# Kernel optimization log

Measured on AMD Instinct MI355X. Metric: run time of the kernel, lower is better.

The kernel has to match this reference:

```python
import jax, jax.numpy as jnp
from jax import lax
import numpy as np

B, L_IN, C_IN, C_MARK = 4, 1024, 7, 4
D, H, DK, DFF, NL = 512, 8, 64, 2048, 4
WINDOW = [4, 4, 4]
INNER = 5


def _get_mask(input_size, window_size, inner_size):
    all_size = [input_size]
    for w in window_size:
        all_size.append(all_size[-1] // w)
    L = sum(all_size)
    m = np.zeros((L, L), dtype=np.float32)
    iw = inner_size // 2
    for li in range(len(all_size)):
        start = sum(all_size[:li])
        for i in range(start, start + all_size[li]):
            m[i, max(i - iw, start):min(i + iw + 1, start + all_size[li])] = 1
    for li in range(1, len(all_size)):
        start = sum(all_size[:li])
        for i in range(start, start + all_size[li]):
            ls = start - all_size[li - 1] + (i - start) * window_size[li - 1]
            if i == start + all_size[li] - 1:
                rs = start
            else:
                rs = start - all_size[li - 1] + (i - start + 1) * window_size[li - 1]
            m[i, ls:rs] = 1
            m[ls:rs, i] = 1
    return (1 - m).astype(bool), all_size


def _refer_points(all_sizes, window_size):
    n = all_sizes[0]
    idx = np.zeros((n, len(all_sizes)), dtype=np.int64)
    for i in range(n):
        idx[i, 0] = i
        former = i
        for j in range(1, len(all_sizes)):
            start = sum(all_sizes[:j])
            inner = former - (start - all_sizes[j - 1])
            former = start + min(inner // window_size[j - 1], all_sizes[j] - 1)
            idx[i, j] = former
    return idx


def _pos_emb(L, d):
    pos = np.arange(L, dtype=np.float32)[:, None]
    div = np.exp(np.arange(0, d, 2, dtype=np.float32) * (-np.log(10000.0) / d))
    pe = np.zeros((L, d), dtype=np.float32)
    pe[:, 0::2] = np.sin(pos * div)
    pe[:, 1::2] = np.cos(pos * div)
    return pe


def _ln(x, g, b, eps=1e-5):
    mu = x.mean(-1, keepdims=True)
    v = ((x - mu) ** 2).mean(-1, keepdims=True)
    return (x - mu) * lax.rsqrt(v + eps) * g + b


def setup_inputs() -> dict:
    key = jax.random.key(0)
    ks = iter(jax.random.split(key, 64))

    def nrm(shape, fan_in):
        return jax.random.normal(next(ks), shape, jnp.float32) / np.float32(np.sqrt(fan_in))

    return dict(
        x_enc=jax.random.normal(next(ks), (B, L_IN, C_IN), jnp.float32),
        x_mark=jax.random.uniform(next(ks), (B, L_IN, C_MARK), jnp.float32),
        conv_w=nrm((D, C_IN, 3), C_IN * 3), conv_b=jnp.zeros((D,), jnp.float32),
        temp_w=nrm((C_MARK, D), C_MARK), temp_b=jnp.zeros((D,), jnp.float32),
        down_w=nrm((D, DK), D), down_b=jnp.zeros((DK,), jnp.float32),
        pyr_conv_w=nrm((3, DK, DK, WINDOW[0]), DK * WINDOW[0]),
        pyr_conv_b=jnp.zeros((3, DK), jnp.float32),
        bn_g=jnp.ones((3, DK), jnp.float32), bn_b=jnp.zeros((3, DK), jnp.float32),
        up_w=nrm((DK, D), DK), up_b=jnp.zeros((D,), jnp.float32),
        norm_g=jnp.ones((D,), jnp.float32), norm_b=jnp.zeros((D,), jnp.float32),
        wq=nrm((NL, D, H * DK), D), wk=nrm((NL, D, H * DK), D), wv=nrm((NL, D, H * DK), D),
        fc_w=nrm((NL, H * DK, D), H * DK), fc_b=jnp.zeros((NL, D), jnp.float32),
        ln1_g=jnp.ones((NL, D), jnp.float32), ln1_b=jnp.zeros((NL, D), jnp.float32),
        w1=nrm((NL, D, DFF), D), b1=jnp.zeros((NL, DFF), jnp.float32),
        w2=nrm((NL, DFF, D), DFF), b2=jnp.zeros((NL, D), jnp.float32),
        ln2_g=jnp.ones((NL, D), jnp.float32), ln2_b=jnp.zeros((NL, D), jnp.float32),
    )


def reference(x_enc, x_mark, conv_w, conv_b, temp_w, temp_b, down_w, down_b,
              pyr_conv_w, pyr_conv_b, bn_g, bn_b, up_w, up_b, norm_g, norm_b,
              wq, wk, wv, fc_w, fc_b, ln1_g, ln1_b, w1, b1, w2, b2, ln2_g, ln2_b):
    mask_np, all_size = _get_mask(L_IN, WINDOW, INNER)
    mask = jnp.asarray(mask_np)                      # (L_tot, L_tot) bool, True = blocked
    idx = jnp.asarray(_refer_points(all_size, WINDOW))  # (L_IN, n_levels)
    pe = jnp.asarray(_pos_emb(L_IN, D))
    L_tot = sum(all_size)

    # --- DataEmbedding: circular Conv1d token emb + positional + temporal linear ---
    xt = jnp.transpose(x_enc, (0, 2, 1))             # (B, C_IN, L)
    xt = jnp.concatenate([xt[:, :, -1:], xt, xt[:, :, :1]], axis=-1)  # circular pad=1
    val = lax.conv_general_dilated(xt, conv_w, (1,), 'VALID',
                                   dimension_numbers=('NCH', 'OIH', 'NCH'))
    val = jnp.transpose(val, (0, 2, 1)) + conv_b
    seq = val + pe[None] + x_mark @ temp_w + temp_b  # (B, L_IN, D); dropout = eval no-op

    # --- Bottleneck_Construct: build pyramid levels with strided convs ---
    tmp = jnp.transpose(seq @ down_w + down_b, (0, 2, 1))  # (B, DK, L_IN)
    outs = []
    for i in range(len(WINDOW)):
        tmp = lax.conv_general_dilated(tmp, pyr_conv_w[i], (WINDOW[i],), 'VALID',
                                       dimension_numbers=('NCH', 'OIH', 'NCH'))
        tmp = tmp + pyr_conv_b[i][None, :, None]
        # BatchNorm1d at eval with running stats (0,1): affine only
        tmp = jax.nn.elu(tmp * bn_g[i][None, :, None] + bn_b[i][None, :, None])
        outs.append(tmp)
    pyr = jnp.transpose(jnp.concatenate(outs, axis=2), (0, 2, 1)) @ up_w + up_b
    seq = _ln(jnp.concatenate([seq, pyr], axis=1), norm_g, norm_b)  # (B, L_tot, D)

    temperature = float(np.sqrt(DK))
    for l in range(NL):
        # post-norm multi-head attention with pyramidal boolean mask
        res = seq
        q = (seq @ wq[l]).reshape(B, L_tot, H, DK)
        k = (seq @ wk[l]).reshape(B, L_tot, H, DK)
        v = (seq @ wv[l]).reshape(B, L_tot, H, DK)
        att = jnp.einsum('bqhd,bkhd->bhqk', q / temperature, k)
        att = jnp.where(mask[None, None], jnp.float32(-1e9), att)
        p = jax.nn.softmax(att, axis=-1)
        o = jnp.einsum('bhqk,bkhd->bqhd', p, v).reshape(B, L_tot, H * DK)
        seq = _ln(o @ fc_w[l] + fc_b[l] + res, ln1_g[l], ln1_b[l])
        # post-norm FFN (exact gelu, as F.gelu)
        res = seq
        hmid = jax.nn.gelu(seq @ w1[l] + b1[l], approximate=False)
        seq = _ln(hmid @ w2[l] + b2[l] + res, ln2_g[l], ln2_b[l])

    # --- refer_points gather: concat all pyramid levels per input position ---
    out = seq[:, idx, :]                             # (B, L_IN, n_levels, D)
    return out.reshape(B, L_IN, -1)                  # (B, L_IN, n_levels*D)
```

## Files before the change

kernel.cpp:

```cpp
#include <hip/hip_runtime.h>
#include <hip/hip_bf16.h>
#include <math.h>


typedef __attribute__((ext_vector_type(8))) short short8;
typedef __attribute__((ext_vector_type(4))) float f32x4;

__device__ inline ushort f2bf(float x) {
  union { __hip_bfloat16 h; ushort u; } cv; cv.h = __float2bfloat16(x); return cv.u;
}
__device__ inline float bf2f(ushort u) {
  union { unsigned int i; float f; } cv; cv.i = (unsigned)u << 16; return cv.f;
}
__device__ inline float lo16(unsigned u) { union { unsigned i; float f; } c; c.i = u << 16; return c.f; }
__device__ inline float hi16(unsigned u) { union { unsigned i; float f; } c; c.i = u & 0xffff0000u; return c.f; }
__device__ inline unsigned pack2(float a, float b) {
  return (unsigned)f2bf(a) | ((unsigned)f2bf(b) << 16);
}

__device__ inline float gelu_f(float x) {
  float y = 0.7978845608028654f * (x + 0.044715f * x * x * x);
  float t = __expf(-2.0f * y);
  float th = (1.0f - t) / (1.0f + t);
  return 0.5f * x * (1.0f + th);
}

__device__ inline int xcd_chunk(int orig, int nwg) {
  int q = nwg >> 3, r = nwg & 7;
  int xcd = orig & 7, idx = orig >> 3;
  int base = (xcd < r) ? xcd * (q + 1) : r * (q + 1) + (xcd - r) * q;
  return base + idx;
}

#define GLD16(gp, lp)                                                        \
  __builtin_amdgcn_global_load_lds(                                          \
      (const __attribute__((address_space(1))) void*)(gp),                   \
      (__attribute__((address_space(3))) void*)(lp), 16, 0, 0)

__global__ __launch_bounds__(512) void embed_kernel(
    const float* __restrict__ x_enc, const float* __restrict__ x_mark,
    const float* __restrict__ conv_w, const float* __restrict__ conv_b,
    const float* __restrict__ temp_w, const float* __restrict__ temp_b,
    float* __restrict__ e, ushort* __restrict__ e_bf) {
  int bl = blockIdx.x;
  int b = bl >> 10, l = bl & 1023;
  int d = threadIdx.x;
  int lm1 = (l + 1023) & 1023;
  int lp1 = (l + 1) & 1023;
  const float* w  = conv_w + d * 21;
  const float* x0 = x_enc + (size_t)(b * 1024 + lm1) * 7;
  const float* x1 = x_enc + (size_t)(b * 1024 + l)   * 7;
  const float* x2 = x_enc + (size_t)(b * 1024 + lp1) * 7;
  float acc = conv_b[d];
#pragma unroll
  for (int ci = 0; ci < 7; ci++) {
    acc = fmaf(x0[ci], w[ci * 3 + 0], acc);
    acc = fmaf(x1[ci], w[ci * 3 + 1], acc);
    acc = fmaf(x2[ci], w[ci * 3 + 2], acc);
  }
  int j = d >> 1;
  float dv = __expf((float)(2 * j) * (-9.210340371976184f / 512.0f));
  float ang = (float)l * dv;
  float pe = (d & 1) ? __cosf(ang) : __sinf(ang);
  const float* xm = x_mark + (size_t)(b * 1024 + l) * 4;
  float mk = temp_b[d];
  mk = fmaf(xm[0], temp_w[d],        mk);
  mk = fmaf(xm[1], temp_w[512 + d],  mk);
  mk = fmaf(xm[2], temp_w[1024 + d], mk);
  mk = fmaf(xm[3], temp_w[1536 + d], mk);
  float v = acc + pe + mk;
  e[(size_t)bl * 512 + d] = v;
  e_bf[(size_t)bl * 512 + d] = f2bf(v);
}

__global__ __launch_bounds__(256) void transpose_cast(
    const float* __restrict__ src, ushort* __restrict__ dst,
    int K, int N, size_t src_lstride, size_t dst_lstride) {
  src += (size_t)blockIdx.z * src_lstride;
  dst += (size_t)blockIdx.z * dst_lstride;
  __shared__ float t[32][33];
  int k0 = blockIdx.y * 32, n0 = blockIdx.x * 32;
  int tx = threadIdx.x, ty = threadIdx.y;
#pragma unroll
  for (int i = 0; i < 4; i++)
    t[ty + i * 8][tx] = src[(size_t)(k0 + ty + i * 8) * N + n0 + tx];
  __syncthreads();
#pragma unroll
  for (int i = 0; i < 4; i++)
    dst[(size_t)(n0 + ty + i * 8) * K + k0 + tx] = f2bf(t[tx][ty + i * 8]);
}

__global__ __launch_bounds__(512, 8) void gemm_bf16_t64w8(
    const ushort* __restrict__ A, const ushort* __restrict__ Bt,
    const float* __restrict__ bias, ushort* __restrict__ C,
    int N, int K, int act) {
  __shared__ short As[2][4096];
  __shared__ short Bs[2][4096];
  int nbx = N >> 6;
  int wgid = xcd_chunk(blockIdx.x, gridDim.x);
  int bx = wgid % nbx, by = wgid / nbx;
  int tid = threadIdx.x;
  int w = tid >> 6, lane = tid & 63;
  int bm = by << 6, bn = bx << 6;
  int gch = (tid & 7) ^ ((tid >> 3) & 7);
  const short* Ab = (const short*)A + (size_t)(bm + (tid >> 3)) * K + gch * 8;
  const short* Bb = (const short*)Bt + (size_t)(bn + (tid >> 3)) * K + gch * 8;
  int ldst = (tid & 448) * 8;
  int wr = (w & 3) << 4, wc = (w >> 2) << 5;
  int lr = lane & 15, kg = lane >> 4;
  int cs0 = ((kg)     ^ (lane & 7)) * 8;
  int cs1 = ((4 + kg) ^ (lane & 7)) * 8;
  f32x4 acc[2] = {};
#define STG(buf, kt) do {                                                    \
    GLD16(Ab + (kt), &As[buf][ldst]);                                        \
    GLD16(Bb + (kt), &Bs[buf][ldst]); } while (0)
  STG(0, 0);
  __syncthreads();
  int nt = K >> 6;
  for (int t = 0; t < nt; t++) {
    int cur = t & 1;
    if (t + 1 < nt) STG(cur ^ 1, (t + 1) << 6);
    short8 a_[2], b_[2][2];
    {
      int rb = (wr + lr) * 64;
      a_[0] = *(const short8*)&As[cur][rb + cs0];
      a_[1] = *(const short8*)&As[cur][rb + cs1];
    }
#pragma unroll
    for (int n = 0; n < 2; n++) {
      int rb = (wc + n * 16 + lr) * 64;
      b_[n][0] = *(const short8*)&Bs[cur][rb + cs0];
      b_[n][1] = *(const short8*)&Bs[cur][rb + cs1];
    }
#pragma unroll
    for (int ks = 0; ks < 2; ks++)
#pragma unroll
      for (int n = 0; n < 2; n++)
        acc[n] = __builtin_amdgcn_mfma_f32_16x16x32_bf16(a_[ks], b_[n][ks], acc[n], 0, 0, 0);
    __syncthreads();
  }
#undef STG
  int r0 = bm + wr + kg * 4;
  int c0 = bn + wc + lr;
#pragma unroll
  for (int n = 0; n < 2; n++) {
    int col = c0 + n * 16;
    float bv = bias ? bias[col] : 0.0f;
#pragma unroll
    for (int j = 0; j < 4; j++) {
      int row = r0 + j;
      float v = acc[n][j] + bv;
      if (act == 1) v = gelu_f(v);
      C[(size_t)row * N + col] = f2bf(v);
    }
  }
}

__global__ __launch_bounds__(256) void gemm_bf16_t32(
    const ushort* __restrict__ A, const ushort* __restrict__ Bt,
    const float* __restrict__ bias, ushort* __restrict__ C,
    int N, int K) {
  __shared__ short As[2][2048];
  __shared__ short Bs[2][4096];
  int nbx = N >> 6;
  int wgid = xcd_chunk(blockIdx.x, gridDim.x);
  int bx = wgid % nbx, by = wgid / nbx;
  int tid = threadIdx.x;
  int w = tid >> 6, lane = tid & 63;
  int bm = by << 5, bn = bx << 6;
  int gch = (tid & 7) ^ ((tid >> 3) & 7);
  const short* Ab = (const short*)A + (size_t)(bm + (tid >> 3)) * K + gch * 8;
  const short* Bb = (const short*)Bt + (size_t)(bn + (tid >> 3)) * K + gch * 8;
  int ldst = (tid & 192) * 8;
  int wr = (w >> 1) << 4, wc = (w & 1) << 5;
  int lr = lane & 15, kg = lane >> 4;
  int cs0 = ((kg)     ^ (lane & 7)) * 8;
  int cs1 = ((4 + kg) ^ (lane & 7)) * 8;
  f32x4 acc[2] = {};
#define STG32(buf, kt) do {                                                  \
    GLD16(Ab + (kt),                  &As[buf][ldst]);                       \
    GLD16(Bb + (kt),                  &Bs[buf][ldst]);                       \
    GLD16(Bb + (kt) + (size_t)32 * K, &Bs[buf][2048 + ldst]); } while (0)
  STG32(0, 0);
  __syncthreads();
  int nt = K >> 6;
  for (int t = 0; t < nt; t++) {
    int cur = t & 1;
    if (t + 1 < nt) STG32(cur ^ 1, (t + 1) << 6);
    short8 a_[2], b_[2][2];
    {
      int rb = (wr + lr) * 64;
      a_[0] = *(const short8*)&As[cur][rb + cs0];
      a_[1] = *(const short8*)&As[cur][rb + cs1];
    }
#pragma unroll
    for (int n = 0; n < 2; n++) {
      int rb = (wc + n * 16 + lr) * 64;
      b_[n][0] = *(const short8*)&Bs[cur][rb + cs0];
      b_[n][1] = *(const short8*)&Bs[cur][rb + cs1];
    }
#pragma unroll
    for (int ks = 0; ks < 2; ks++)
#pragma unroll
      for (int n = 0; n < 2; n++)
        acc[n] = __builtin_amdgcn_mfma_f32_16x16x32_bf16(a_[ks], b_[n][ks], acc[n], 0, 0, 0);
    __syncthreads();
  }
#undef STG32
  int r0 = bm + wr + kg * 4;
  int c0 = bn + wc + lr;
#pragma unroll
  for (int n = 0; n < 2; n++) {
    int col = c0 + n * 16;
    float bv = bias ? bias[col] : 0.0f;
#pragma unroll
    for (int j = 0; j < 4; j++) {
      int row = r0 + j;
      C[(size_t)row * N + col] = f2bf(acc[n][j] + bv);
    }
  }
}

__global__ __launch_bounds__(64) void pyr_conv(
    const ushort* __restrict__ in, int in_base, int in_bstr,
    ushort* __restrict__ out, int out_base, int out_bstr, int out_len,
    const float* __restrict__ w, const float* __restrict__ bias,
    const float* __restrict__ bng, const float* __restrict__ bnb) {
  int blk = blockIdx.x;
  int b = blk / out_len, to = blk - b * out_len;
  int co = threadIdx.x;
  __shared__ float xin[4][64];
  const ushort* src = in + (size_t)(b * in_bstr + in_base + 4 * to) * 64;
#pragma unroll
  for (int r2 = 0; r2 < 4; r2++) xin[r2][co] = bf2f(src[r2 * 64 + co]);
  __syncthreads();
  const float* wr = w + (size_t)co * 256;
  float acc = bias[co];
#pragma unroll 16
  for (int ci = 0; ci < 64; ci++) {
    acc = fmaf(xin[0][ci], wr[ci * 4 + 0], acc);
    acc = fmaf(xin[1][ci], wr[ci * 4 + 1], acc);
    acc = fmaf(xin[2][ci], wr[ci * 4 + 2], acc);
    acc = fmaf(xin[3][ci], wr[ci * 4 + 3], acc);
  }
  float y = fmaf(bng[co], acc, bnb[co]);
  y = y > 0.0f ? y : expm1f(y);
  out[(size_t)(b * out_bstr + out_base + to) * 64 + co] = f2bf(y);
}

__global__ __launch_bounds__(256) void ln_concat(
    const float* __restrict__ e, const ushort* __restrict__ pyru,
    const float* __restrict__ g, const float* __restrict__ bta,
    ushort* __restrict__ seq_bf) {
  int r = (blockIdx.x << 2) + (threadIdx.x >> 6);
  int lane = threadIdx.x & 63;
  int b = r / 1360, i = r - b * 1360;
  int c = lane << 3;
  float v[8];
  if (i < 1024) {
    const float* src = e + (size_t)(b * 1024 + i) * 512 + c;
    float4 v0 = *(const float4*)&src[0];
    float4 v1 = *(const float4*)&src[4];
    v[0] = v0.x; v[1] = v0.y; v[2] = v0.z; v[3] = v0.w;
    v[4] = v1.x; v[5] = v1.y; v[6] = v1.z; v[7] = v1.w;
  } else {
    uint4 sv = *(const uint4*)(pyru + (size_t)(b * 336 + (i - 1024)) * 512 + c);
    v[0] = lo16(sv.x); v[1] = hi16(sv.x); v[2] = lo16(sv.y); v[3] = hi16(sv.y);
    v[4] = lo16(sv.z); v[5] = hi16(sv.z); v[6] = lo16(sv.w); v[7] = hi16(sv.w);
  }
  float sum = v[0]+v[1]+v[2]+v[3]+v[4]+v[5]+v[6]+v[7];
#pragma unroll
  for (int off = 1; off < 64; off <<= 1) sum += __shfl_xor(sum, off);
  float mu = sum * (1.0f / 512.0f);
  float sq = 0.0f;
#pragma unroll
  for (int k = 0; k < 8; k++) { v[k] -= mu; sq += v[k] * v[k]; }
#pragma unroll
  for (int off = 1; off < 64; off <<= 1) sq += __shfl_xor(sq, off);
  float inv = rsqrtf(sq * (1.0f / 512.0f) + 1e-5f);
  float4 g0 = *(const float4*)&g[c],   g1 = *(const float4*)&g[c + 4];
  float4 b0 = *(const float4*)&bta[c], b1 = *(const float4*)&bta[c + 4];
  uint4 pk;
  pk.x = pack2(v[0]*inv*g0.x + b0.x, v[1]*inv*g0.y + b0.y);
  pk.y = pack2(v[2]*inv*g0.z + b0.z, v[3]*inv*g0.w + b0.w);
  pk.z = pack2(v[4]*inv*g1.x + b1.x, v[5]*inv*g1.y + b1.y);
  pk.w = pack2(v[6]*inv*g1.z + b1.z, v[7]*inv*g1.w + b1.w);
  *(uint4*)(seq_bf + (size_t)r * 512 + c) = pk;
}

__global__ __launch_bounds__(256) void ln_add(
    ushort* __restrict__ seq_bf, const ushort* __restrict__ t1,
    const float* __restrict__ g, const float* __restrict__ bta) {
  int r = (blockIdx.x << 2) + (threadIdx.x >> 6);
  int lane = threadIdx.x & 63;
  int c = lane << 3;
  ushort* row = seq_bf + (size_t)r * 512 + c;
  uint4 sv = *(const uint4*)row;
  uint4 tv = *(const uint4*)(t1 + (size_t)r * 512 + c);
  float v[8] = {
    lo16(sv.x) + lo16(tv.x), hi16(sv.x) + hi16(tv.x),
    lo16(sv.y) + lo16(tv.y), hi16(sv.y) + hi16(tv.y),
    lo16(sv.z) + lo16(tv.z), hi16(sv.z) + hi16(tv.z),
    lo16(sv.w) + lo16(tv.w), hi16(sv.w) + hi16(tv.w) };
  float sum = v[0]+v[1]+v[2]+v[3]+v[4]+v[5]+v[6]+v[7];
#pragma unroll
  for (int off = 1; off < 64; off <<= 1) sum += __shfl_xor(sum, off);
  float mu = sum * (1.0f / 512.0f);
  float sq = 0.0f;
#pragma unroll
  for (int k = 0; k < 8; k++) { v[k] -= mu; sq += v[k] * v[k]; }
#pragma unroll
  for (int off = 1; off < 64; off <<= 1) sq += __shfl_xor(sq, off);
  float inv = rsqrtf(sq * (1.0f / 512.0f) + 1e-5f);
  float4 g0 = *(const float4*)&g[c],   g1 = *(const float4*)&g[c + 4];
  float4 b0 = *(const float4*)&bta[c], b1 = *(const float4*)&bta[c + 4];
  uint4 pk;
  pk.x = pack2(v[0]*inv*g0.x + b0.x, v[1]*inv*g0.y + b0.y);
  pk.y = pack2(v[2]*inv*g0.z + b0.z, v[3]*inv*g0.w + b0.w);
  pk.z = pack2(v[4]*inv*g1.x + b1.x, v[5]*inv*g1.y + b1.y);
  pk.w = pack2(v[6]*inv*g1.z + b1.z, v[7]*inv*g1.w + b1.w);
  *(uint4*)row = pk;
}

__global__ __launch_bounds__(512) void attn_sparse(
    const ushort* __restrict__ qkv, ushort* __restrict__ o) {
  int r = blockIdx.x;
  int b = r / 1360, i = r - b * 1360;
  int h = threadIdx.x >> 6, lane = threadIdx.x & 63;
  int S, sz, li;
  if (i < 1024)      { li = 0; S = 0;    sz = 1024; }
  else if (i < 1280) { li = 1; S = 1024; sz = 256; }
  else if (i < 1344) { li = 2; S = 1280; sz = 64; }
  else               { li = 3; S = 1344; sz = 16; }
  int p = i - S;
  int lo = p - 2; if (lo < 0) lo = 0;
  int hi = p + 2; if (hi > sz - 1) hi = sz - 1;
  int cnt = hi - lo + 1;
  int nk = cnt + (li > 0 ? 4 : 0) + (li < 3 ? 1 : 0);
  int Sprev = (li == 1) ? 0 : (li == 2) ? 1024 : 1280;
  int Snext = (li == 0) ? 1024 : (li == 1) ? 1280 : 1344;
  int j2 = lane >> 2, c = lane & 3;
  int key;
  if (j2 < cnt)                      key = S + lo + j2;
  else if (li > 0 && j2 - cnt < 4)   key = Sprev + 4 * p + (j2 - cnt);
  else if (li < 3)                   key = Snext + (p >> 2);
  else                               key = S + p;
  float partial = 0.0f;
  {
    const uint4* qv = (const uint4*)(qkv + (size_t)r * 1536 + h * 64 + c * 16);
    const uint4* kv = (const uint4*)(qkv + (size_t)(b * 1360 + key) * 1536 + 512 + h * 64 + c * 16);
#pragma unroll
    for (int cc = 0; cc < 2; cc++) {
      uint4 a = qv[cc], k4 = kv[cc];
      partial = fmaf(lo16(a.x), lo16(k4.x), partial); partial = fmaf(hi16(a.x), hi16(k4.x), partial);
      partial = fmaf(lo16(a.y), lo16(k4.y), partial); partial = fmaf(hi16(a.y), hi16(k4.y), partial);
      partial = fmaf(lo16(a.z), lo16(k4.z), partial); partial = fmaf(hi16(a.z), hi16(k4.z), partial);
      partial = fmaf(lo16(a.w), lo16(k4.w), partial); partial = fmaf(hi16(a.w), hi16(k4.w), partial);
    }
  }
  partial += __shfl_xor(partial, 1);
  partial += __shfl_xor(partial, 2);
  float s = (j2 < nk) ? partial * 0.125f : -1e30f;
  float m = s;
  m = fmaxf(m, __shfl_xor(m, 4));
  m = fmaxf(m, __shfl_xor(m, 8));
  m = fmaxf(m, __shfl_xor(m, 16));
  m = fmaxf(m, __shfl_xor(m, 32));
  float ev = __expf(s - m);
  float den = ev;
  den += __shfl_xor(den, 4);
  den += __shfl_xor(den, 8);
  den += __shfl_xor(den, 16);
  den += __shfl_xor(den, 32);
  float inv = 1.0f / den;
  float acc = 0.0f;
  for (int j = 0; j < nk; j++) {
    float pj = __shfl(ev, 4 * j) * inv;
    int kj = __shfl(key, 4 * j);
    float vv = bf2f(qkv[(size_t)(b * 1360 + kj) * 1536 + 1024 + h * 64 + lane]);
    acc = fmaf(pj, vv, acc);
  }
  o[(size_t)r * 512 + h * 64 + lane] = f2bf(acc);
}

__global__ __launch_bounds__(512) void gather_out(
    const ushort* __restrict__ seq_bf, float* __restrict__ out) {
  int bl = blockIdx.x;
  int b = bl >> 10, i = bl & 1023;
  int t = threadIdx.x;
  int q = t >> 7, e4 = (t & 127) << 2;
  int src_row = (q == 0) ? i
              : (q == 1) ? 1024 + (i >> 2)
              : (q == 2) ? 1280 + (i >> 4)
              :            1344 + (i >> 6);
  size_t base = (size_t)b * 1360;
  const ushort* sp = seq_bf + ((base + src_row) * 512 + e4);
  uint2 sv = *(const uint2*)sp;
  float4 ov;
  ov.x = lo16(sv.x); ov.y = hi16(sv.x);
  ov.z = lo16(sv.y); ov.w = hi16(sv.y);
  *(float4*)&out[(size_t)bl * 2048 + q * 512 + e4] = ov;
}

extern "C" void kernel_launch(void* const* d_in, const int* in_sizes, int n_in,
                              void* d_out, int out_size, void* d_ws, size_t ws_size,
                              hipStream_t stream) {
  const float* x_enc   = (const float*)d_in[0];
  const float* x_mark  = (const float*)d_in[1];
  const float* conv_w  = (const float*)d_in[2];
  const float* conv_b  = (const float*)d_in[3];
  const float* temp_w  = (const float*)d_in[4];
  const float* temp_b  = (const float*)d_in[5];
  const float* down_w  = (const float*)d_in[6];
  const float* down_b  = (const float*)d_in[7];
  const float* pyr_w   = (const float*)d_in[8];
  const float* pyr_b   = (const float*)d_in[9];
  const float* bn_g    = (const float*)d_in[10];
  const float* bn_b    = (const float*)d_in[11];
  const float* up_w    = (const float*)d_in[12];
  const float* up_b    = (const float*)d_in[13];
  const float* norm_g  = (const float*)d_in[14];
  const float* norm_b  = (const float*)d_in[15];
  const float* wq      = (const float*)d_in[16];
  const float* wk      = (const float*)d_in[17];
  const float* wv      = (const float*)d_in[18];
  const float* fc_w    = (const float*)d_in[19];
  const float* fc_b    = (const float*)d_in[20];
  const float* ln1_g   = (const float*)d_in[21];
  const float* ln1_b   = (const float*)d_in[22];
  const float* w1      = (const float*)d_in[23];
  const float* b1      = (const float*)d_in[24];
  const float* w2      = (const float*)d_in[25];
  const float* b2      = (const float*)d_in[26];
  const float* ln2_g   = (const float*)d_in[27];
  const float* ln2_b   = (const float*)d_in[28];

  float* ws = (float*)d_ws;
  float*  e       = ws;
  ushort* e_bf    = (ushort*)(ws + 2097152);
  ushort* tmp0_bf = (ushort*)(ws + 3145728);
  ushort* pyrf_bf = (ushort*)(ws + 3276800);
  ushort* pyru_bf = (ushort*)(ws + 3319808);
  ushort* qkv_bf = (ushort*)ws;
  ushort* o_bf   = (ushort*)(ws + 4227072);
  ushort* th_bf  = (ushort*)ws;
  ushort* t1     = (ushort*)(ws + 5636096);
  ushort* dwt    = (ushort*)(ws + 7045120);
  ushort* uwt    = (ushort*)(ws + 7061504);
  ushort* seq_bf = (ushort*)(ws + 11272192);
  ushort* qkvw   = (ushort*)(ws + 12681216);
  ushort* fcw    = (ushort*)(ws + 14254080);
  ushort* w1t    = (ushort*)(ws + 14778368);
  ushort* w2t    = (ushort*)(ws + 16875520);

  dim3 tb(32, 8);
  transpose_cast<<<dim3(16, 16, 4), tb, 0, stream>>>(wq, qkvw,          512, 512,  262144, 786432);
  transpose_cast<<<dim3(16, 16, 4), tb, 0, stream>>>(wk, qkvw + 262144, 512, 512,  262144, 786432);
  transpose_cast<<<dim3(16, 16, 4), tb, 0, stream>>>(wv, qkvw + 524288, 512, 512,  262144, 786432);
  transpose_cast<<<dim3(16, 16, 4), tb, 0, stream>>>(fc_w, fcw,         512, 512,  262144, 262144);
  transpose_cast<<<dim3(64, 16, 4), tb, 0, stream>>>(w1, w1t,           512, 2048, 1048576, 1048576);
  transpose_cast<<<dim3(16, 64, 4), tb, 0, stream>>>(w2, w2t,           2048, 512, 1048576, 1048576);
  transpose_cast<<<dim3(2, 16, 1), tb, 0, stream>>>(down_w, dwt,        512, 64,   0, 0);
  transpose_cast<<<dim3(16, 2, 1), tb, 0, stream>>>(up_w, uwt,          64, 512,   0, 0);

  embed_kernel<<<4096, 512, 0, stream>>>(x_enc, x_mark, conv_w, conv_b,
                                         temp_w, temp_b, e, e_bf);
  gemm_bf16_t32<<<128, 256, 0, stream>>>(e_bf, dwt, down_b, tmp0_bf, 64, 512);
  pyr_conv<<<4 * 256, 64, 0, stream>>>(tmp0_bf, 0, 1024, pyrf_bf, 0, 336, 256,
                                       pyr_w, pyr_b, bn_g, bn_b);
  pyr_conv<<<4 * 64, 64, 0, stream>>>(pyrf_bf, 0, 336, pyrf_bf, 256, 336, 64,
                                      pyr_w + 16384, pyr_b + 64, bn_g + 64, bn_b + 64);
  pyr_conv<<<4 * 16, 64, 0, stream>>>(pyrf_bf, 256, 336, pyrf_bf, 320, 336, 16,
                                      pyr_w + 32768, pyr_b + 128, bn_g + 128, bn_b + 128);
  gemm_bf16_t32<<<8 * 42, 256, 0, stream>>>(pyrf_bf, uwt, up_b, pyru_bf, 512, 64);
  ln_concat<<<1360, 256, 0, stream>>>(e, pyru_bf, norm_g, norm_b, seq_bf);

  for (int l = 0; l < 4; l++) {
    gemm_bf16_t64w8<<<24 * 86, 512, 0, stream>>>(seq_bf, qkvw + (size_t)l * 786432,
                                                 nullptr, qkv_bf, 1536, 512, 0);
    attn_sparse<<<5440, 512, 0, stream>>>(qkv_bf, o_bf);
    gemm_bf16_t32<<<8 * 172, 256, 0, stream>>>(o_bf, fcw + (size_t)l * 262144,
                                               fc_b + l * 512, t1, 512, 512);
    ln_add<<<1360, 256, 0, stream>>>(seq_bf, t1, ln1_g + l * 512, ln1_b + l * 512);
    gemm_bf16_t64w8<<<32 * 86, 512, 0, stream>>>(seq_bf, w1t + (size_t)l * 1048576,
                                                 b1 + l * 2048, th_bf, 2048, 512, 1);
    gemm_bf16_t32<<<8 * 172, 256, 0, stream>>>(th_bf, w2t + (size_t)l * 1048576,
                                               b2 + l * 512, t1, 512, 2048);
    ln_add<<<1360, 256, 0, stream>>>(seq_bf, t1, ln2_g + l * 512, ln2_b + l * 512);
  }
  gather_out<<<4096, 512, 0, stream>>>(seq_bf, (float*)d_out);
}
```

Measured before the change: 521.3 us.

## Fuse final LayerNorm with output gather, drop fp32 embed buffer, merge transposes

The last FFN LayerNorm now writes fp32 results straight into the gathered output layout, replicating pyramid rows, so the separate gather kernel goes away. The embedding kernel no longer stores an fp32 copy, and ln_concat reads the bf16 embedding instead, which cuts memory traffic. The four square weight transposes become one launch. The LayerNorm input for the fine level is now rounded to bf16 first, and the final output is written in fp32 from LN values before bf16 rounding, so numerics shift slightly.

Result: slower. 574.4 us (+10.2%).

```diff
diff --git a/kernel.cpp b/kernel.cpp
--- a/kernel.cpp
+++ b/kernel.cpp
@@ -41,7 +41,7 @@
     const float* __restrict__ x_enc, const float* __restrict__ x_mark,
     const float* __restrict__ conv_w, const float* __restrict__ conv_b,
     const float* __restrict__ temp_w, const float* __restrict__ temp_b,
-    float* __restrict__ e, ushort* __restrict__ e_bf) {
+    ushort* __restrict__ e_bf) {
   int bl = blockIdx.x;
   int b = bl >> 10, l = bl & 1023;
   int d = threadIdx.x;
@@ -68,9 +68,7 @@
   mk = fmaf(xm[1], temp_w[512 + d],  mk);
   mk = fmaf(xm[2], temp_w[1024 + d], mk);
   mk = fmaf(xm[3], temp_w[1536 + d], mk);
-  float v = acc + pe + mk;
-  e[(size_t)bl * 512 + d] = v;
-  e_bf[(size_t)bl * 512 + d] = f2bf(v);
+  e_bf[(size_t)bl * 512 + d] = f2bf(acc + pe + mk);
 }
 
 __global__ __launch_bounds__(256) void transpose_cast(
@@ -88,6 +86,28 @@
 #pragma unroll
   for (int i = 0; i < 4; i++)
     dst[(size_t)(n0 + ty + i * 8) * K + k0 + tx] = f2bf(t[tx][ty + i * 8]);
+}
+
+__global__ __launch_bounds__(256) void transpose_cast_sq(
+    const float* __restrict__ wq, const float* __restrict__ wk,
+    const float* __restrict__ wv, const float* __restrict__ fw,
+    ushort* __restrict__ qkvw, ushort* __restrict__ fcw) {
+  int z = blockIdx.z;
+  int kind = z >> 2, layer = z & 3;
+  const float* src = ((kind == 0) ? wq : (kind == 1) ? wk : (kind == 2) ? wv : fw)
+                     + (size_t)layer * 262144;
+  ushort* dst = (kind < 3) ? qkvw + (size_t)layer * 786432 + (size_t)kind * 262144
+                           : fcw + (size_t)layer * 262144;
+  __shared__ float t[32][33];
+  int k0 = blockIdx.y * 32, n0 = blockIdx.x * 32;
+  int tx = threadIdx.x, ty = threadIdx.y;
+#pragma unroll
+  for (int i = 0; i < 4; i++)
+    t[ty + i * 8][tx] = src[(size_t)(k0 + ty + i * 8) * 512 + n0 + tx];
+  __syncthreads();
+#pragma unroll
+  for (int i = 0; i < 4; i++)
+    dst[(size_t)(n0 + ty + i * 8) * 512 + k0 + tx] = f2bf(t[tx][ty + i * 8]);
 }
 
 __global__ __launch_bounds__(512, 8) void gemm_bf16_t64w8(
@@ -249,25 +269,19 @@
 }
 
 __global__ __launch_bounds__(256) void ln_concat(
-    const float* __restrict__ e, const ushort* __restrict__ pyru,
+    const ushort* __restrict__ e_bf, const ushort* __restrict__ pyru,
     const float* __restrict__ g, const float* __restrict__ bta,
     ushort* __restrict__ seq_bf) {
   int r = (blockIdx.x << 2) + (threadIdx.x >> 6);
   int lane = threadIdx.x & 63;
   int b = r / 1360, i = r - b * 1360;
   int c = lane << 3;
-  float v[8];
-  if (i < 1024) {
-    const float* src = e + (size_t)(b * 1024 + i) * 512 + c;
-    float4 v0 = *(const float4*)&src[0];
-    float4 v1 = *(const float4*)&src[4];
-    v[0] = v0.x; v[1] = v0.y; v[2] = v0.z; v[3] = v0.w;
-    v[4] = v1.x; v[5] = v1.y; v[6] = v1.z; v[7] = v1.w;
-  } else {
-    uint4 sv = *(const uint4*)(pyru + (size_t)(b * 336 + (i - 1024)) * 512 + c);
-    v[0] = lo16(sv.x); v[1] = hi16(sv.x); v[2] = lo16(sv.y); v[3] = hi16(sv.y);
-    v[4] = lo16(sv.z); v[5] = hi16(sv.z); v[6] = lo16(sv.w); v[7] = hi16(sv.w);
-  }
+  const ushort* src = (i < 1024)
+      ? (e_bf + (size_t)(b * 1024 + i) * 512)
+      : (pyru + (size_t)(b * 336 + (i - 1024)) * 512);
+  uint4 sv = *(const uint4*)(src + c);
+  float v[8] = { lo16(sv.x), hi16(sv.x), lo16(sv.y), hi16(sv.y),
+                 lo16(sv.z), hi16(sv.z), lo16(sv.w), hi16(sv.w) };
   float sum = v[0]+v[1]+v[2]+v[3]+v[4]+v[5]+v[6]+v[7];
 #pragma unroll
   for (int off = 1; off < 64; off <<= 1) sum += __shfl_xor(sum, off);
@@ -320,6 +334,50 @@
   pk.z = pack2(v[4]*inv*g1.x + b1.x, v[5]*inv*g1.y + b1.y);
   pk.w = pack2(v[6]*inv*g1.z + b1.z, v[7]*inv*g1.w + b1.w);
   *(uint4*)row = pk;
+}
+
+__global__ __launch_bounds__(256) void ln_add_out(
+    const ushort* __restrict__ seq_bf, const ushort* __restrict__ t1,
+    const float* __restrict__ g, const float* __restrict__ bta,
+    float* __restrict__ out) {
+  int r = (blockIdx.x << 2) + (threadIdx.x >> 6);
+  int lane = threadIdx.x & 63;
+  int b = r / 1360, i = r - b * 1360;
+  int c = lane << 3;
+  uint4 sv = *(const uint4*)(seq_bf + (size_t)r * 512 + c);
+  uint4 tv = *(const uint4*)(t1 + (size_t)r * 512 + c);
+  float v[8] = {
+    lo16(sv.x) + lo16(tv.x), hi16(sv.x) + hi16(tv.x),
+    lo16(sv.y) + lo16(tv.y), hi16(sv.y) + hi16(tv.y),
+    lo16(sv.z) + lo16(tv.z), hi16(sv.z) + hi16(tv.z),
+    lo16(sv.w) + lo16(tv.w), hi16(sv.w) + hi16(tv.w) };
+  float sum = v[0]+v[1]+v[2]+v[3]+v[4]+v[5]+v[6]+v[7];
+#pragma unroll
+  for (int off = 1; off < 64; off <<= 1) sum += __shfl_xor(sum, off);
+  float mu = sum * (1.0f / 512.0f);
+  float sq = 0.0f;
+#pragma unroll
+  for (int k = 0; k < 8; k++) { v[k] -= mu; sq += v[k] * v[k]; }
+#pragma unroll
+  for (int off = 1; off < 64; off <<= 1) sq += __shfl_xor(sq, off);
+  float inv = rsqrtf(sq * (1.0f / 512.0f) + 1e-5f);
+  float4 g0 = *(const float4*)&g[c],   g1 = *(const float4*)&g[c + 4];
+  float4 b0 = *(const float4*)&bta[c], b1 = *(const float4*)&bta[c + 4];
+  float4 o0 = make_float4(v[0]*inv*g0.x + b0.x, v[1]*inv*g0.y + b0.y,
+                          v[2]*inv*g0.z + b0.z, v[3]*inv*g0.w + b0.w);
+  float4 o1 = make_float4(v[4]*inv*g1.x + b1.x, v[5]*inv*g1.y + b1.y,
+                          v[6]*inv*g1.z + b1.z, v[7]*inv*g1.w + b1.w);
+  int p, q, rep;
+  if (i < 1024)      { p = i;        q = 0; rep = 1; }
+  else if (i < 1280) { p = i - 1024; q = 1; rep = 4; }
+  else if (i < 1344) { p = i - 1280; q = 2; rep = 16; }
+  else               { p = i - 1344; q = 3; rep = 64; }
+  int i0 = p * rep;
+  for (int t = 0; t < rep; t++) {
+    float* dst = out + ((size_t)(b * 1024 + i0 + t) * 2048 + q * 512 + c);
+    *(float4*)&dst[0] = o0;
+    *(float4*)&dst[4] = o1;
+  }
 }
 
 __global__ __launch_bounds__(512) void attn_sparse(
@@ -381,25 +439,6 @@
     acc = fmaf(pj, vv, acc);
   }
   o[(size_t)r * 512 + h * 64 + lane] = f2bf(acc);
-}
-
-__global__ __launch_bounds__(512) void gather_out(
-    const ushort* __restrict__ seq_bf, float* __restrict__ out) {
-  int bl = blockIdx.x;
-  int b = bl >> 10, i = bl & 1023;
-  int t = threadIdx.x;
-  int q = t >> 7, e4 = (t & 127) << 2;
-  int src_row = (q == 0) ? i
-              : (q == 1) ? 1024 + (i >> 2)
-              : (q == 2) ? 1280 + (i >> 4)
-              :            1344 + (i >> 6);
-  size_t base = (size_t)b * 1360;
-  const ushort* sp = seq_bf + ((base + src_row) * 512 + e4);
-  uint2 sv = *(const uint2*)sp;
-  float4 ov;
-  ov.x = lo16(sv.x); ov.y = hi16(sv.x);
-  ov.z = lo16(sv.y); ov.w = hi16(sv.y);
-  *(float4*)&out[(size_t)bl * 2048 + q * 512 + e4] = ov;
 }
 
 extern "C" void kernel_launch(void* const* d_in, const int* in_sizes, int n_in,
@@ -436,11 +475,10 @@
   const float* ln2_b   = (const float*)d_in[28];
 
   float* ws = (float*)d_ws;
-  float*  e       = ws;
-  ushort* e_bf    = (ushort*)(ws + 2097152);
-  ushort* tmp0_bf = (ushort*)(ws + 3145728);
-  ushort* pyrf_bf = (ushort*)(ws + 3276800);
-  ushort* pyru_bf = (ushort*)(ws + 3319808);
+  ushort* e_bf    = (ushort*)ws;
+  ushort* tmp0_bf = (ushort*)(ws + 1048576);
+  ushort* pyrf_bf = (ushort*)(ws + 1179648);
+  ushort* pyru_bf = (ushort*)(ws + 1222656);
   ushort* qkv_bf = (ushort*)ws;
   ushort* o_bf   = (ushort*)(ws + 4227072);
   ushort* th_bf  = (ushort*)ws;
@@ -454,17 +492,14 @@
   ushort* w2t    = (ushort*)(ws + 16875520);
 
   dim3 tb(32, 8);
-  transpose_cast<<<dim3(16, 16, 4), tb, 0, stream>>>(wq, qkvw,          512, 512,  262144, 786432);
-  transpose_cast<<<dim3(16, 16, 4), tb, 0, stream>>>(wk, qkvw + 262144, 512, 512,  262144, 786432);
-  transpose_cast<<<dim3(16, 16, 4), tb, 0, stream>>>(wv, qkvw + 524288, 512, 512,  262144, 786432);
-  transpose_cast<<<dim3(16, 16, 4), tb, 0, stream>>>(fc_w, fcw,         512, 512,  262144, 262144);
-  transpose_cast<<<dim3(64, 16, 4), tb, 0, stream>>>(w1, w1t,           512, 2048, 1048576, 1048576);
-  transpose_cast<<<dim3(16, 64, 4), tb, 0, stream>>>(w2, w2t,           2048, 512, 1048576, 1048576);
-  transpose_cast<<<dim3(2, 16, 1), tb, 0, stream>>>(down_w, dwt,        512, 64,   0, 0);
-  transpose_cast<<<dim3(16, 2, 1), tb, 0, stream>>>(up_w, uwt,          64, 512,   0, 0);
+  transpose_cast_sq<<<dim3(16, 16, 16), tb, 0, stream>>>(wq, wk, wv, fc_w, qkvw, fcw);
+  transpose_cast<<<dim3(64, 16, 4), tb, 0, stream>>>(w1, w1t, 512, 2048, 1048576, 1048576);
+  transpose_cast<<<dim3(16, 64, 4), tb, 0, stream>>>(w2, w2t, 2048, 512, 1048576, 1048576);
+  transpose_cast<<<dim3(2, 16, 1), tb, 0, stream>>>(down_w, dwt, 512, 64, 0, 0);
+  transpose_cast<<<dim3(16, 2, 1), tb, 0, stream>>>(up_w, uwt, 64, 512, 0, 0);
 
   embed_kernel<<<4096, 512, 0, stream>>>(x_enc, x_mark, conv_w, conv_b,
-                                         temp_w, temp_b, e, e_bf);
+                                         temp_w, temp_b, e_bf);
   gemm_bf16_t32<<<128, 256, 0, stream>>>(e_bf, dwt, down_b, tmp0_bf, 64, 512);
   pyr_conv<<<4 * 256, 64, 0, stream>>>(tmp0_bf, 0, 1024, pyrf_bf, 0, 336, 256,
                                        pyr_w, pyr_b, bn_g, bn_b);
@@ -473,7 +508,7 @@
   pyr_conv<<<4 * 16, 64, 0, stream>>>(pyrf_bf, 256, 336, pyrf_bf, 320, 336, 16,
                                       pyr_w + 32768, pyr_b + 128, bn_g + 128, bn_b + 128);
   gemm_bf16_t32<<<8 * 42, 256, 0, stream>>>(pyrf_bf, uwt, up_b, pyru_bf, 512, 64);
-  ln_concat<<<1360, 256, 0, stream>>>(e, pyru_bf, norm_g, norm_b, seq_bf);
+  ln_concat<<<1360, 256, 0, stream>>>(e_bf, pyru_bf, norm_g, norm_b, seq_bf);
 
   for (int l = 0; l < 4; l++) {
     gemm_bf16_t64w8<<<24 * 86, 512, 0, stream>>>(seq_bf, qkvw + (size_t)l * 786432,
@@ -486,7 +521,11 @@
                                                  b1 + l * 2048, th_bf, 2048, 512, 1);
     gemm_bf16_t32<<<8 * 172, 256, 0, stream>>>(th_bf, w2t + (size_t)l * 1048576,
                                                b2 + l * 512, t1, 512, 2048);
-    ln_add<<<1360, 256, 0, stream>>>(seq_bf, t1, ln2_g + l * 512, ln2_b + l * 512);
-  }
-  gather_out<<<4096, 512, 0, stream>>>(seq_bf, (float*)d_out);
-}
+    if (l < 3) {
+      ln_add<<<1360, 256, 0, stream>>>(seq_bf, t1, ln2_g + l * 512, ln2_b + l * 512);
+    } else {
+      ln_add_out<<<1360, 256, 0, stream>>>(seq_bf, t1, ln2_g + l * 512,
+                                           ln2_b + l * 512, (float*)d_out);
+    }
+  }
+}
```
